# Kernel optimization log

Hardware: AMD Instinct MI355X
Metric: run time of the kernel (lower is better)

## Reference

```python
import jax, jax.numpy as jnp
import numpy as np

B, T, C_IN, H, W = 4, 3, 64, 64, 64
E = 96            # embed_dim
K = 3             # patch_size / deformable kernel size
PAD = 1
N = K * K         # 9 sampled positions per pixel
TOPK = 2
DG = 8            # deformable groups


def conv3x3(x, w, b):
    y = jax.lax.conv_general_dilated(x, w, (1, 1), ((1, 1), (1, 1)),
                                     dimension_numbers=('NCHW', 'OIHW', 'NCHW'))
    return y + b[None, :, None, None]


def lrelu(x):
    return jnp.where(x >= 0, x, 0.1 * x)


def deform_sample(x, off_feat, om_w, om_b):
    """DSP_sep2: modulated deformable sampling. Returns (B, C, N, H, W)."""
    B_, C, H_, W_ = x.shape
    om = conv3x3(off_feat, om_w, om_b).reshape(B_, 3, DG, N, H_, W_)
    off_y, off_x, mask = om[:, 0], om[:, 1], jax.nn.sigmoid(om[:, 2])  # (B,DG,N,H,W)
    ky = (jnp.arange(N) // K - PAD).astype(x.dtype)
    kx = (jnp.arange(N) % K - PAD).astype(x.dtype)
    py = off_y + ky[None, None, :, None, None] + jnp.arange(H_, dtype=x.dtype)[None, None, None, :, None]
    px = off_x + kx[None, None, :, None, None] + jnp.arange(W_, dtype=x.dtype)[None, None, None, None, :]
    y0 = jnp.floor(py); x0 = jnp.floor(px)
    wy = py - y0;       wx = px - x0
    xg = x.reshape(B_, DG, C // DG, H_, W_)
    gat = jax.vmap(jax.vmap(lambda xg_, yi, xi: xg_[:, yi, xi]))  # -> (B,DG,Cg,N,H,W)

    def corner(yc, xc, wgt):
        valid = ((yc >= 0) & (yc < H_) & (xc >= 0) & (xc < W_)).astype(x.dtype)
        yi = jnp.clip(yc, 0, H_ - 1).astype(jnp.int32)
        xi = jnp.clip(xc, 0, W_ - 1).astype(jnp.int32)
        return gat(xg, yi, xi) * (wgt * valid)[:, :, None]

    out = (corner(y0,     x0,     (1 - wy) * (1 - wx)) +
           corner(y0,     x0 + 1, (1 - wy) * wx) +
           corner(y0 + 1, x0,     wy * (1 - wx)) +
           corner(y0 + 1, x0 + 1, wy * wx))
    out = out * mask[:, :, None]  # modulation
    return out.reshape(B_, C, N, H_, W_)


def deform_attn(q, k, v, oc1_w, oc1_b, oc2_w, oc2_b, om_w, om_b):
    B_, E_, H_, W_ = q.shape
    HW = H_ * W_
    off = lrelu(conv3x3(jnp.concatenate([q, k], axis=1), oc1_w, oc1_b))
    off = lrelu(conv3x3(off, oc2_w, oc2_b))
    ko = deform_sample(k, off, om_w, om_b).transpose(0, 3, 4, 2, 1).reshape(B_, HW, N, E_)
    vo = deform_sample(v, off, om_w, om_b).transpose(0, 3, 4, 2, 1).reshape(B_, HW, N, E_)
    qr = q.reshape(B_, E_, HW).transpose(0, 2, 1)              # (B,HW,E)
    rel = jnp.einsum('bpne,bpe->bpn', ko, qr)                  # (B,HW,N)
    vals, idx = jax.lax.top_k(rel, TOPK)                       # (B,HW,k)
    corr = jax.nn.softmax(vals, axis=-1)
    idx_e = jnp.broadcast_to(idx[..., None], idx.shape + (E_,))
    ksel = jnp.take_along_axis(ko, idx_e, axis=2)              # (B,HW,k,E)
    vsel = jnp.take_along_axis(vo, idx_e, axis=2)
    k_up = jnp.einsum('bpke,bpk->bpe', ksel, corr)
    w_ori = jnp.einsum('bpe,bpe->bp', qr, k_up)                # (B,HW)
    v_re = jnp.einsum('bpke,bpk->bpe', vsel, corr).transpose(0, 2, 1)  # (B,E,HW)
    return w_ori, v_re


def setup_inputs() -> dict:
    key = jax.random.key(0)
    ks = jax.random.split(key, 18)
    s = 0.05
    return {
        'fea_full_map': jax.random.normal(ks[0], (B, T, C_IN, H, W), jnp.float32),
        'cf_w': s * jax.random.normal(ks[1], (E, C_IN, 3, 3), jnp.float32),
        'cf_b': s * jax.random.normal(ks[2], (E,), jnp.float32),
        'wq':   s * jax.random.normal(ks[3], (E, E), jnp.float32),
        'bq':   s * jax.random.normal(ks[4], (E,), jnp.float32),
        'wk':   s * jax.random.normal(ks[5], (E, E), jnp.float32),
        'bk':   s * jax.random.normal(ks[6], (E,), jnp.float32),
        'wv':   s * jax.random.normal(ks[7], (E, E), jnp.float32),
        'bv':   s * jax.random.normal(ks[8], (E,), jnp.float32),
        'oc1_w': s * jax.random.normal(ks[9], (E, 2 * E, 3, 3), jnp.float32),
        'oc1_b': s * jax.random.normal(ks[10], (E,), jnp.float32),
        'oc2_w': s * jax.random.normal(ks[11], (E, E, 3, 3), jnp.float32),
        'oc2_b': s * jax.random.normal(ks[12], (E,), jnp.float32),
        'om_w': 0.01 * jax.random.normal(ks[13], (DG * 3 * N, E, 3, 3), jnp.float32),
        'om_b': 0.01 * jax.random.normal(ks[14], (DG * 3 * N,), jnp.float32),
        'cl_w': s * jax.random.normal(ks[15], (C_IN, E, 3, 3), jnp.float32),
        'cl_b': s * jax.random.normal(ks[16], (C_IN,), jnp.float32),
    }


def reference(fea_full_map, cf_w, cf_b, wq, bq, wk, bk, wv, bv,
              oc1_w, oc1_b, oc2_w, oc2_b, om_w, om_b, cl_w, cl_b):
    B_, T_, C_, H_, W_ = fea_full_map.shape
    x = fea_full_map.reshape(B_ * T_, C_, H_, W_)
    emb = conv3x3(x, cf_w, cf_b).reshape(B_, T_, E, H_, W_)
    # per-frame linear Q/K/V over the channel dim (nn.Linear: y = x W^T + b)
    q = jnp.einsum('btchw,dc->btdhw', emb, wq) + bq[None, None, :, None, None]
    k = jnp.einsum('btchw,dc->btdhw', emb, wk) + bk[None, None, :, None, None]
    v = jnp.einsum('btchw,dc->btdhw', emb, wv) + bv[None, None, :, None, None]
    feats = []
    for jj in range(T_):
        ws, vs = [], []
        for ii in range(T_):
            if ii != jj:
                w_, v_ = deform_attn(q[:, jj], k[:, ii], v[:, ii],
                                     oc1_w, oc1_b, oc2_w, oc2_b, om_w, om_b)
                ws.append(w_); vs.append(v_)
        wm = jax.nn.softmax(jnp.stack(ws, axis=1), axis=1)  # (B, T-1, HW)
        vm = jnp.stack(vs, axis=1)                          # (B, T-1, E, HW)
        feats.append((vm * wm[:, :, None, :]).sum(axis=1).reshape(B_, E, H_, W_))
    f = jnp.stack(feats, axis=1).reshape(B_ * T_, E, H_, W_)
    out = conv3x3(f, cl_w, cl_b)
    return out + x
```

## Files before the change

### kernel.cpp

```cpp
#include <hip/hip_runtime.h>
#include <math.h>

#define PIXN 4096

typedef _Float16 f16;
typedef short s16x8 __attribute__((ext_vector_type(8)));
typedef unsigned short u16x4 __attribute__((ext_vector_type(4)));
typedef float f32x4 __attribute__((ext_vector_type(4)));

__device__ __forceinline__ f16 f2h(float f) { return (f16)f; }
__device__ __forceinline__ float h2f(f16 h) { return (float)h; }

__device__ __forceinline__ unsigned short f2bf(float f) {
  unsigned u = __float_as_uint(f);
  u += 0x7fffu + ((u >> 16) & 1u);
  return (unsigned short)(u >> 16);
}
__device__ __forceinline__ float bf2f(unsigned short h) {
  return __uint_as_float(((unsigned)h) << 16);
}

enum { ACT_NONE = 0, ACT_LRELU = 1, ACT_SIG144 = 2 };
enum { IN_FLAT = 1, IN_UVPAIR = 2, IN_QKV = 3, IN_BF = 4 };
enum { OUT_FLAT = 0, OUT_NCHWRES = 1 };

__device__ __forceinline__ void wprep_mfma(const float* __restrict__ w, unsigned short* __restrict__ dst,
                                           int srcCIN, int cinOff, int COUTv, int COUTP,
                                           int total, int idx) {
  if (idx >= total) return;
  int e = idx & 7;
  int t = idx >> 3;
  int co = t % COUTP; t /= COUTP;
  int kch = t & 3; t >>= 2;
  int KCv = srcCIN == 64 ? 2 : 3;
  (void)KCv;
  int kc = t % 3;
  int tap = t / 3;
  int ci = kc * 32 + kch * 8 + e;
  float v = 0.f;
  if (co < COUTv) v = w[((long)co * srcCIN + cinOff + ci) * 9 + tap];
  unsigned short h = f2bf(v);
  dst[idx] = h;
  dst[total + idx] = f2bf(v - bf2f(h));
}

__global__ __launch_bounds__(256) void prep_all(
    const float* __restrict__ cf_w, const float* __restrict__ oc1_w,
    const float* __restrict__ oc2_w, const float* __restrict__ om_w,
    const float* __restrict__ cl_w,
    const float* __restrict__ wq, const float* __restrict__ wk, const float* __restrict__ wv,
    const float* __restrict__ bq, const float* __restrict__ bk, const float* __restrict__ bv,
    const float* __restrict__ cf_b,
    unsigned short* __restrict__ WBQ, float* __restrict__ BQ,
    unsigned short* __restrict__ WB1, unsigned short* __restrict__ WB2,
    unsigned short* __restrict__ WB3, unsigned short* __restrict__ WB4) {
  int idx = blockIdx.x * 256 + threadIdx.x;
  switch (blockIdx.y) {
    case 0: {
      if (idx < 288) {
        int m = idx / 96, ep = idx % 96;
        const float* wm = (m == 0) ? wq : (m == 1) ? wk : wv;
        const float* bm = (m == 0) ? bq : (m == 1) ? bk : bv;
        float s = bm[ep];
        for (int c = 0; c < 96; ++c) s = fmaf(wm[ep * 96 + c], cf_b[c], s);
        BQ[idx] = s;
      }
      if (idx < 165888) {
        int e = idx & 7;
        int t = idx >> 3;
        int co = t % 288; t /= 288;
        int kch = t & 3; t >>= 2;
        int kc = t & 1, tap = t >> 1;
        int ci = kc * 32 + kch * 8 + e;
        int m = co / 96, ep = co % 96;
        const float* wm = (m == 0) ? wq : (m == 1) ? wk : wv;
        float s = 0.f;
        for (int c = 0; c < 96; ++c)
          s = fmaf(wm[ep * 96 + c], cf_w[((long)c * 64 + ci) * 9 + tap], s);
        unsigned short h = f2bf(s);
        WBQ[idx] = h;
        WBQ[165888 + idx] = f2bf(s - bf2f(h));
      }
      break;
    }
    case 1: wprep_mfma(oc1_w, WB1, 192, 0, 96, 96, 82944, idx); break;
    case 2: wprep_mfma(oc1_w, WB1 + 2 * 82944, 192, 96, 96, 96, 82944, idx); break;
    case 3: wprep_mfma(oc2_w, WB2, 96, 0, 96, 96, 82944, idx); break;
    case 4: wprep_mfma(om_w, WB3, 96, 0, 216, 224, 193536, idx); break;
    default: wprep_mfma(cl_w, WB4, 96, 0, 64, 64, 55296, idx); break;
  }
}

__global__ __launch_bounds__(256) void nchw2bf(const float* __restrict__ fea,
                                               unsigned short* __restrict__ hi,
                                               unsigned short* __restrict__ lo) {
  const int y = blockIdx.x;
  const int img = blockIdx.y;
  const int t = threadIdx.x;
  const int x = t & 63, cg = t >> 6;
  __shared__ unsigned short sh[64][68], sl[64][68];
  const float* base = fea + ((long)img * 64) * PIXN + y * 64;
#pragma unroll
  for (int k = 0; k < 16; ++k) {
    int ci = cg * 16 + k;
    float v = base[(long)ci * PIXN + x];
    unsigned short h = f2bf(v);
    sh[x][ci] = h;
    sl[x][ci] = f2bf(v - bf2f(h));
  }
  __syncthreads();
  const long ob = (long)img * PIXN + y * 64;
  for (int i = t; i < 2048; i += 256) {
    int plane = i >> 10;
    int r = i & 1023;
    int px = r >> 4, q4 = r & 15;
    u16x4 v4 = *reinterpret_cast<const u16x4*>(plane ? &sl[px][q4 * 4] : &sh[px][q4 * 4]);
    unsigned short* dst = (plane ? lo : hi) + (ob + px) * 64 + q4 * 4;
    *reinterpret_cast<u16x4*>(dst) = v4;
  }
}

template <int CIN, int COUT, int COUTW, int NCOG, int IMODE, int ACT, int OMODE>
__global__ __launch_bounds__(512, 4) void conv3x3r(
    const float* __restrict__ in, const float* __restrict__ in2,
    const float* __restrict__ bias_in,
    const unsigned short* __restrict__ WB,
    const float* __restrict__ bias,
    float* __restrict__ out,
    const float* __restrict__ resid) {
  constexpr int KC = CIN / 32;
  constexpr int COG = COUTW / NCOG;
  constexpr int NTW = COG / 32;
  constexpr int AST = 4 * 66 * 8 + 8;
  constexpr int APL = 4 * AST;
  constexpr int BSTEP = COUTW * 32;
  constexpr int TOTB = 9 * KC * BSTEP;

  __shared__ __align__(16) unsigned short Abuf[2 * APL];

  const int tid = threadIdx.x;
  const int lane = tid & 63;
  const int wid = tid >> 6;
  const int wm = wid & 3;
  const int wn = wid >> 2;
  const int iz = blockIdx.y;
  const int y0 = blockIdx.x * 2;
  const int zoff = (NCOG > 1) ? blockIdx.z * COG : 0;

  const float* baseA = nullptr;
  const float* baseB2 = nullptr;
  const unsigned short* hpl = nullptr;
  const unsigned short* lpl = nullptr;
  const unsigned short* wbe = WB;
  int LDV = CIN;
  if constexpr (IMODE == IN_UVPAIR) {
    int pair = iz >> 2, b = iz & 3;
    int jj = pair >> 1, rr2 = pair & 1;
    int ii = (rr2 == 0) ? (jj == 0 ? 1 : 0) : (jj == 2 ? 1 : 2);
    baseA = in + (long)(b * 3 + jj) * (PIXN * 96);
    baseB2 = in2 + (long)(b * 3 + ii) * (PIXN * 96);
    LDV = 96;
  } else if constexpr (IMODE == IN_QKV) {
    int sel = iz / 12, img = iz % 12;
    baseA = in + (long)img * (PIXN * 288) + sel * 96;
    wbe = WB + (long)sel * (2 * TOTB);
    LDV = 288;
  } else if constexpr (IMODE == IN_BF) {
    hpl = reinterpret_cast<const unsigned short*>(in) + (long)iz * (PIXN * 64);
    lpl = reinterpret_cast<const unsigned short*>(in2) + (long)iz * (PIXN * 64);
  } else {
    baseA = in + (long)iz * ((long)PIXN * CIN);
    LDV = CIN;
  }

  auto stageA = [&](int kc) {
    if constexpr (IMODE == IN_BF) {
      for (int i = tid; i < 4 * 66 * 4; i += 512) {
        int ci8 = i & 3;
        int t = i >> 2;
        int xp = t % 66, rr = t / 66;
        int y = y0 + rr - 1, x = xp - 1;
        s16x8 hv = {0, 0, 0, 0, 0, 0, 0, 0};
        s16x8 lv = {0, 0, 0, 0, 0, 0, 0, 0};
        if ((unsigned)y < 64u && (unsigned)x < 64u) {
          long off = (long)(y * 64 + x) * 64 + kc * 32 + ci8 * 8;
          hv = *reinterpret_cast<const s16x8*>(hpl + off);
          lv = *reinterpret_cast<const s16x8*>(lpl + off);
        }
        int base = ci8 * AST + (rr * 66 + xp) * 8;
        *reinterpret_cast<s16x8*>(&Abuf[base]) = hv;
        *reinterpret_cast<s16x8*>(&Abuf[APL + base]) = lv;
      }
    } else {
      for (int i = tid; i < 4 * 66 * 8; i += 512) {
        int ci4 = i & 7;
        int t = i >> 3;
        int xp = t % 66, rr = t / 66;
        int y = y0 + rr - 1, x = xp - 1;
        float4 v = make_float4(0.f, 0.f, 0.f, 0.f);
        if ((unsigned)y < 64u && (unsigned)x < 64u) {
          long off = (long)(y * 64 + x) * LDV + kc * 32 + ci4 * 4;
          if constexpr (IMODE == IN_UVPAIR) {
            float4 u = *reinterpret_cast<const float4*>(baseA + off);
            float4 w2 = *reinterpret_cast<const float4*>(baseB2 + off);
            float4 bi = *reinterpret_cast<const float4*>(bias_in + kc * 32 + ci4 * 4);
            v.x = u.x + w2.x + bi.x; v.x = v.x >= 0.f ? v.x : 0.1f * v.x;
            v.y = u.y + w2.y + bi.y; v.y = v.y >= 0.f ? v.y : 0.1f * v.y;
            v.z = u.z + w2.z + bi.z; v.z = v.z >= 0.f ? v.z : 0.1f * v.z;
            v.w = u.w + w2.w + bi.w; v.w = v.w >= 0.f ? v.w : 0.1f * v.w;
          } else {
            v = *reinterpret_cast<const float4*>(baseA + off);
          }
        }
        unsigned short h0 = f2bf(v.x), h1 = f2bf(v.y), h2 = f2bf(v.z), h3 = f2bf(v.w);
        u16x4 hv = {h0, h1, h2, h3};
        u16x4 lv = {f2bf(v.x - bf2f(h0)), f2bf(v.y - bf2f(h1)),
                    f2bf(v.z - bf2f(h2)), f2bf(v.w - bf2f(h3))};
        int base = (ci4 >> 1) * AST + (rr * 66 + xp) * 8 + (ci4 & 1) * 4;
        *reinterpret_cast<u16x4*>(&Abuf[base]) = hv;
        *reinterpret_cast<u16x4*>(&Abuf[APL + base]) = lv;
      }
    }
  };

  f32x4 acc[2][NTW];
#pragma unroll
  for (int nt = 0; nt < NTW; ++nt) {
    int co = zoff + (wn * NTW + nt) * 16 + (lane & 15);
    float b0 = 0.f;
    if (bias != nullptr && co < COUT) b0 = bias[co];
#pragma unroll
    for (int mt2 = 0; mt2 < 2; ++mt2) {
      acc[mt2][nt][0] = b0; acc[mt2][nt][1] = b0;
      acc[mt2][nt][2] = b0; acc[mt2][nt][3] = b0;
    }
  }

  stageA(0);
  __syncthreads();

  const int blo = ((lane >> 4) * COUTW + zoff + (wn * NTW) * 16 + (lane & 15)) * 8;

  s16x8 b0h, b0l, b1h, b1l;
  {
    const unsigned short* p = wbe + blo;
    b0h = *reinterpret_cast<const s16x8*>(p);
    b0l = *reinterpret_cast<const s16x8*>(p + TOTB);
  }

  long bo = 0;
#pragma unroll 1
  for (int kc = 0; kc < KC; ++kc) {
#pragma unroll 1
    for (int tap = 0; tap < 9; ++tap) {
      const int dy = tap / 3, dx = tap % 3;
      const long bo_next = (tap < 8) ? bo + (long)KC * BSTEP
                                     : ((kc + 1 < KC) ? (long)(kc + 1) * BSTEP : 0);

      s16x8 ah[2], al[2];
      {
        int ci8 = lane >> 4;
        int m = lane & 15;
#pragma unroll
        for (int mt2 = 0; mt2 < 2; ++mt2) {
          int px = (wm * 2 + mt2) * 16 + m;
          int r = px >> 6, x = px & 63;
          int aoff = ci8 * AST + ((r + dy) * 66 + (x + dx)) * 8;
          ah[mt2] = *reinterpret_cast<const s16x8*>(&Abuf[aoff]);
          al[mt2] = *reinterpret_cast<const s16x8*>(&Abuf[APL + aoff]);
        }
      }

#pragma unroll
      for (int nt = 0; nt < NTW; ++nt) {
        const long nboff = (nt + 1 < NTW) ? (bo + (long)(nt + 1) * 128) : bo_next;
        const unsigned short* np = wbe + nboff + blo;
        if ((nt & 1) == 0) {
          b1h = *reinterpret_cast<const s16x8*>(np);
          b1l = *reinterpret_cast<const s16x8*>(np + TOTB);
        } else {
          b0h = *reinterpret_cast<const s16x8*>(np);
          b0l = *reinterpret_cast<const s16x8*>(np + TOTB);
        }
        const s16x8 bh = (nt & 1) ? b1h : b0h;
        const s16x8 bl = (nt & 1) ? b1l : b0l;
#pragma unroll
        for (int mt2 = 0; mt2 < 2; ++mt2) {
          acc[mt2][nt] = __builtin_amdgcn_mfma_f32_16x16x32_bf16(ah[mt2], bh, acc[mt2][nt], 0, 0, 0);
          acc[mt2][nt] = __builtin_amdgcn_mfma_f32_16x16x32_bf16(al[mt2], bh, acc[mt2][nt], 0, 0, 0);
          acc[mt2][nt] = __builtin_amdgcn_mfma_f32_16x16x32_bf16(ah[mt2], bl, acc[mt2][nt], 0, 0, 0);
        }
      }
      if constexpr (NTW & 1) {
        b0h = b1h; b0l = b1l;
      }
      bo = bo_next;
    }
    if (kc + 1 < KC) {
      __syncthreads();
      stageA(kc + 1);
      __syncthreads();
    }
  }

#pragma unroll
  for (int mt2 = 0; mt2 < 2; ++mt2) {
#pragma unroll
    for (int nt = 0; nt < NTW; ++nt) {
      int co = zoff + (wn * NTW + nt) * 16 + (lane & 15);
      if (COUTW > COUT && co >= COUT) continue;
#pragma unroll
      for (int r = 0; r < 4; ++r) {
        int px = (wm * 2 + mt2) * 16 + (lane >> 4) * 4 + r;
        float v = acc[mt2][nt][r];
        if constexpr (ACT == ACT_LRELU) v = v >= 0.f ? v : 0.1f * v;
        if constexpr (ACT == ACT_SIG144) {
          if (co >= 144) v = 1.f / (1.f + expf(-v));
        }
        if constexpr (OMODE == OUT_FLAT) {
          const long obase = (long)iz * PIXN + blockIdx.x * 128;
          out[(obase + px) * COUT + co] = v;
        } else {
          long oo = (long)iz * ((long)COUT * PIXN) + (long)co * PIXN + blockIdx.x * 128 + px;
          out[oo] = v + resid[oo];
        }
      }
    }
  }
}

#define CWSLOT 580
__global__ __launch_bounds__(256) void attn3_k(const float* __restrict__ qkv,
                                               const float* __restrict__ om,
                                               float* __restrict__ w_buf,
                                               f16* __restrict__ vre) {
  const int pair = blockIdx.y;
  const int jj = pair >> 1, rr = pair & 1;
  const int ii = (rr == 0) ? (jj == 0 ? 1 : 0) : (jj == 2 ? 1 : 2);
  const int wv = threadIdx.x >> 6;
  const int lane = threadIdx.x & 63;
  const int bp0 = blockIdx.x * 8 + wv * 2;

  __shared__ float s_om[8 * 216];
  __shared__ float s_cw[8 * CWSLOT];

  {
    const float* omrow = om + ((long)pair * 16384 + bp0) * 216;
    float* dst = s_om + wv * 432;
    for (int i = lane; i < 432; i += 64) dst[i] = omrow[i];
  }
  __syncthreads();

  for (int t = lane; t < 144; t += 64) {
    int ph = t / 72, cmb = t - ph * 72;
    int g = cmb / 9, n = cmb - g * 9;
    int p = (bp0 + ph) & 4095;
    int y = p >> 6, x = p & 63;
    const float* so = s_om + (wv * 2 + ph) * 216;
    float oy = so[g * 9 + n], ox = so[72 + g * 9 + n], m = so[144 + g * 9 + n];
    float py = oy + (float)(y + n / 3 - 1);
    float px = ox + (float)(x + n % 3 - 1);
    float y0f = floorf(py), x0f = floorf(px);
    float wy = py - y0f, wx = px - x0f;
    float* dst = s_cw + (wv * 2 + ph) * CWSLOT + cmb * 8;
#pragma unroll
    for (int dy = 0; dy < 2; ++dy) {
#pragma unroll
      for (int dx = 0; dx < 2; ++dx) {
        float yc = y0f + dy, xc = x0f + dx;
        bool valid = (yc >= 0.f) & (yc < 64.f) & (xc >= 0.f) & (xc < 64.f);
        float w = (dy ? wy : 1.f - wy) * (dx ? wx : 1.f - wx) * m;
        w = valid ? w : 0.f;
        int yi = (int)fminf(fmaxf(yc, 0.f), 63.f);
        int xi = (int)fminf(fmaxf(xc, 0.f), 63.f);
        int idx = (yi * 64 + xi) * 288 + 96;
        dst[dy * 2 + dx] = w;
        dst[4 + dy * 2 + dx] = __int_as_float(idx);
      }
    }
  }
  __syncthreads();

  const int ph = lane >> 5;
  const int li = lane & 31;
  const int bp = bp0 + ph;
  const int b = bp >> 12;
  const int cb = li * 3;
  const int g = li >> 2;
  const float* kimg = qkv + (long)(b * 3 + ii) * (PIXN * 288);
  const float* qrow = qkv + ((long)(b * 3 + jj) * PIXN + (bp & 4095)) * 288 + cb;
  const float q0 = qrow[0], q1 = qrow[1], q2 = qrow[2];
  const float* cw = s_cw + (wv * 2 + ph) * CWSLOT + g * 9 * 8;

  float ka[9][3];
  float rel[9];
#pragma unroll
  for (int n = 0; n < 9; ++n) {
    float4 w4 = *reinterpret_cast<const float4*>(cw + n * 8);
    float4 i4 = *reinterpret_cast<const float4*>(cw + n * 8 + 4);
    int ia = __float_as_int(i4.x) + cb, ib = __float_as_int(i4.y) + cb;
    int ic = __float_as_int(i4.z) + cb, id = __float_as_int(i4.w) + cb;
#pragma unroll
    for (int j = 0; j < 3; ++j) {
      float a = w4.x * kimg[ia + j];
      a = fmaf(w4.y, kimg[ib + j], a);
      a = fmaf(w4.z, kimg[ic + j], a);
      a = fmaf(w4.w, kimg[id + j], a);
      ka[n][j] = a;
    }
    float part = q0 * ka[n][0];
    part = fmaf(q1, ka[n][1], part);
    part = fmaf(q2, ka[n][2], part);
#pragma unroll
    for (int off = 16; off > 0; off >>= 1) part += __shfl_xor(part, off, 64);
    rel[n] = part;
  }

  int i0 = 0; float v0 = rel[0];
  float ks0a = ka[0][0], ks0b = ka[0][1], ks0c = ka[0][2];
#pragma unroll
  for (int n = 1; n < 9; ++n) {
    bool t = rel[n] > v0;
    v0 = t ? rel[n] : v0; i0 = t ? n : i0;
    ks0a = t ? ka[n][0] : ks0a; ks0b = t ? ka[n][1] : ks0b; ks0c = t ? ka[n][2] : ks0c;
  }
  int i1 = 0; float v1 = -3.4e38f;
  float ks1a = 0.f, ks1b = 0.f, ks1c = 0.f;
#pragma unroll
  for (int n = 0; n < 9; ++n) {
    bool t = (n != i0) && rel[n] > v1;
    v1 = t ? rel[n] : v1; i1 = t ? n : i1;
    ks1a = t ? ka[n][0] : ks1a; ks1b = t ? ka[n][1] : ks1b; ks1c = t ? ka[n][2] : ks1c;
  }
  float e = expf(v1 - v0);
  float cw0 = 1.f / (1.f + e), cw1 = e * cw0;

  float wpart = q0 * (cw0 * ks0a + cw1 * ks1a);
  wpart = fmaf(q1, cw0 * ks0b + cw1 * ks1b, wpart);
  wpart = fmaf(q2, cw0 * ks0c + cw1 * ks1c, wpart);
#pragma unroll
  for (int off = 16; off > 0; off >>= 1) wpart += __shfl_xor(wpart, off, 64);
  if (li == 0) w_buf[(long)pair * 16384 + bp] = wpart;

  float4 wA = *reinterpret_cast<const float4*>(cw + i0 * 8);
  float4 iA = *reinterpret_cast<const float4*>(cw + i0 * 8 + 4);
  float4 wB = *reinterpret_cast<const float4*>(cw + i1 * 8);
  float4 iB = *reinterpret_cast<const float4*>(cw + i1 * 8 + 4);
  int a0 = __float_as_int(iA.x) + 96 + cb, a1 = __float_as_int(iA.y) + 96 + cb;
  int a2 = __float_as_int(iA.z) + 96 + cb, a3 = __float_as_int(iA.w) + 96 + cb;
  int b0 = __float_as_int(iB.x) + 96 + cb, b1 = __float_as_int(iB.y) + 96 + cb;
  int b2 = __float_as_int(iB.z) + 96 + cb, b3 = __float_as_int(iB.w) + 96 + cb;
  f16* vrow = vre + ((long)pair * 16384 + bp) * 96 + cb;
#pragma unroll
  for (int j = 0; j < 3; ++j) {
    float va = wA.x * kimg[a0 + j];
    va = fmaf(wA.y, kimg[a1 + j], va);
    va = fmaf(wA.z, kimg[a2 + j], va);
    va = fmaf(wA.w, kimg[a3 + j], va);
    float vb = wB.x * kimg[b0 + j];
    vb = fmaf(wB.y, kimg[b1 + j], vb);
    vb = fmaf(wB.z, kimg[b2 + j], vb);
    vb = fmaf(wB.w, kimg[b3 + j], vb);
    vrow[j] = f2h(cw0 * va + cw1 * vb);
  }
}

__global__ __launch_bounds__(256) void merge_k(const float* __restrict__ w_buf,
                                               const f16* __restrict__ vre,
                                               float* __restrict__ f_t) {
  long idx = (long)blockIdx.x * 256 + threadIdx.x;
  const long TOT = (long)4 * 3 * PIXN * 24;
  if (idx >= TOT) return;
  int c4 = idx % 24;
  long t = idx / 24;
  int p = t % PIXN;
  long t2 = t / PIXN;
  int jj = t2 % 3;
  int b = (int)(t2 / 3);
  long bpi = (long)b * PIXN + p;
  int pr0 = jj * 2, pr1 = jj * 2 + 1;
  float w0 = w_buf[(long)pr0 * 16384 + bpi];
  float w1 = w_buf[(long)pr1 * 16384 + bpi];
  float mx = fmaxf(w0, w1);
  float e0 = expf(w0 - mx), e1 = expf(w1 - mx);
  float inv = 1.f / (e0 + e1);
  float s0 = e0 * inv, s1 = e1 * inv;
  const f16* va = &vre[((long)pr0 * 16384 + bpi) * 96 + c4 * 4];
  const f16* vb = &vre[((long)pr1 * 16384 + bpi) * 96 + c4 * 4];
  float4 r;
  r.x = s0 * h2f(va[0]) + s1 * h2f(vb[0]);
  r.y = s0 * h2f(va[1]) + s1 * h2f(vb[1]);
  r.z = s0 * h2f(va[2]) + s1 * h2f(vb[2]);
  r.w = s0 * h2f(va[3]) + s1 * h2f(vb[3]);
  *reinterpret_cast<float4*>(f_t + ((long)(b * 3 + jj) * PIXN + p) * 96 + c4 * 4) = r;
}

extern "C" void kernel_launch(void* const* d_in, const int* in_sizes, int n_in,
                              void* d_out, int out_size, void* d_ws, size_t ws_size,
                              hipStream_t stream) {
  const float* fea = (const float*)d_in[0];
  const float* cf_w = (const float*)d_in[1];
  const float* cf_b = (const float*)d_in[2];
  const float* wq = (const float*)d_in[3];
  const float* bq = (const float*)d_in[4];
  const float* wk = (const float*)d_in[5];
  const float* bk = (const float*)d_in[6];
  const float* wv = (const float*)d_in[7];
  const float* bv = (const float*)d_in[8];
  const float* oc1_w = (const float*)d_in[9];
  const float* oc1_b = (const float*)d_in[10];
  const float* oc2_w = (const float*)d_in[11];
  const float* oc2_b = (const float*)d_in[12];
  const float* om_w = (const float*)d_in[13];
  const float* om_b = (const float*)d_in[14];
  const float* cl_w = (const float*)d_in[15];
  const float* cl_b = (const float*)d_in[16];

  char* base = (char*)d_ws;
  size_t o = 0;
  auto carve = [&](size_t bytes) { char* p = base + o; o += (bytes + 255) & ~255UL; return p; };

  unsigned short* WBQ = (unsigned short*)carve(2UL * 165888 * 2);
  float* BQ = (float*)carve(288UL * 4);
  unsigned short* WB1 = (unsigned short*)carve(2UL * 2 * 82944 * 2);
  unsigned short* WB2 = (unsigned short*)carve(2UL * 82944 * 2);
  unsigned short* WB3 = (unsigned short*)carve(2UL * 193536 * 2);
  unsigned short* WB4 = (unsigned short*)carve(2UL * 55296 * 2);
  unsigned short* feaH = (unsigned short*)carve(12UL * PIXN * 64 * 2);
  unsigned short* feaL = (unsigned short*)carve(12UL * PIXN * 64 * 2);

  float* om_t = (float*)carve(21233664UL * 4);
  float* qkv_t = (float*)carve(14155776UL * 4);
  float* U_t = (float*)carve(4718592UL * 4);
  float* V_t = (float*)carve(4718592UL * 4);
  float* off2_t = (float*)carve(9437184UL * 4);
  float* w_buf = (float*)carve(98304UL * 4);
  float* f_t = U_t;
  f16* vre_b = (f16*)V_t;

  prep_all<<<dim3(756, 6), 256, 0, stream>>>(cf_w, oc1_w, oc2_w, om_w, cl_w,
                                             wq, wk, wv, bq, bk, bv, cf_b,
                                             WBQ, BQ, WB1, WB2, WB3, WB4);

  nchw2bf<<<dim3(64, 12), 256, 0, stream>>>(fea, feaH, feaL);

  conv3x3r<64, 288, 288, 3, IN_BF, ACT_NONE, OUT_FLAT><<<dim3(32, 12, 3), 512, 0, stream>>>(
      (const float*)feaH, (const float*)feaL, nullptr, WBQ, BQ, qkv_t, nullptr);

  conv3x3r<96, 96, 96, 1, IN_QKV, ACT_NONE, OUT_FLAT><<<dim3(32, 24, 1), 512, 0, stream>>>(
      qkv_t, nullptr, nullptr, WB1, nullptr, U_t, nullptr);

  conv3x3r<96, 96, 96, 1, IN_UVPAIR, ACT_LRELU, OUT_FLAT><<<dim3(32, 24, 1), 512, 0, stream>>>(
      U_t, V_t, oc1_b, WB2, oc2_b, off2_t, nullptr);

  conv3x3r<96, 216, 224, 1, IN_FLAT, ACT_SIG144, OUT_FLAT><<<dim3(32, 24, 1), 512, 0, stream>>>(
      off2_t, nullptr, nullptr, WB3, om_b, om_t, nullptr);

  attn3_k<<<dim3(2048, 6), 256, 0, stream>>>(qkv_t, om_t, w_buf, vre_b);
  merge_k<<<4608, 256, 0, stream>>>(w_buf, vre_b, f_t);

  conv3x3r<96, 64, 64, 1, IN_FLAT, ACT_NONE, OUT_NCHWRES><<<dim3(32, 12, 1), 512, 0, stream>>>(
      f_t, nullptr, nullptr, WB4, cl_b, (float*)d_out, fea);
}
```

Measured before the change: 515.9 us.

## Parameterize conv warp layout and split offset-mask conv across output-channel groups

Adds a WN template parameter that sets how the 8 waves split pixels versus output channels, so each wave handles WN pixel tiles and a matching number of channel tiles. Weight fragments for the next tap are now prefetched into a per-tile register array for the whole tap instead of ping-ponging one tile ahead. The offset/mask conv pads its output channels to 256, splits them into two z-groups and uses a 4x4 wave layout, doubling its grid so more blocks run concurrently. The costs are extra padded weight traffic and more registers for the prefetched B fragments, which could lower occupancy.

```diff
diff --git a/kernel.cpp b/kernel.cpp
--- a/kernel.cpp
+++ b/kernel.cpp
@@ -32,8 +32,6 @@
   int t = idx >> 3;
   int co = t % COUTP; t /= COUTP;
   int kch = t & 3; t >>= 2;
-  int KCv = srcCIN == 64 ? 2 : 3;
-  (void)KCv;
   int kc = t % 3;
   int tap = t / 3;
   int ci = kc * 32 + kch * 8 + e;
@@ -86,7 +84,7 @@
     case 1: wprep_mfma(oc1_w, WB1, 192, 0, 96, 96, 82944, idx); break;
     case 2: wprep_mfma(oc1_w, WB1 + 2 * 82944, 192, 96, 96, 96, 82944, idx); break;
     case 3: wprep_mfma(oc2_w, WB2, 96, 0, 96, 96, 82944, idx); break;
-    case 4: wprep_mfma(om_w, WB3, 96, 0, 216, 224, 193536, idx); break;
+    case 4: wprep_mfma(om_w, WB3, 96, 0, 216, 256, 221184, idx); break;
     default: wprep_mfma(cl_w, WB4, 96, 0, 64, 64, 55296, idx); break;
   }
 }
@@ -120,7 +118,7 @@
   }
 }
 
-template <int CIN, int COUT, int COUTW, int NCOG, int IMODE, int ACT, int OMODE>
+template <int CIN, int COUT, int COUTW, int NCOG, int IMODE, int ACT, int OMODE, int WN>
 __global__ __launch_bounds__(512, 4) void conv3x3r(
     const float* __restrict__ in, const float* __restrict__ in2,
     const float* __restrict__ bias_in,
@@ -129,8 +127,10 @@
     float* __restrict__ out,
     const float* __restrict__ resid) {
   constexpr int KC = CIN / 32;
+  constexpr int WM = 8 / WN;
+  constexpr int MT = WN;
   constexpr int COG = COUTW / NCOG;
-  constexpr int NTW = COG / 32;
+  constexpr int NTW = COG / (WN * 16);
   constexpr int AST = 4 * 66 * 8 + 8;
   constexpr int APL = 4 * AST;
   constexpr int BSTEP = COUTW * 32;
@@ -141,8 +141,8 @@
   const int tid = threadIdx.x;
   const int lane = tid & 63;
   const int wid = tid >> 6;
-  const int wm = wid & 3;
-  const int wn = wid >> 2;
+  const int wm = wid % WM;
+  const int wn = wid / WM;
   const int iz = blockIdx.y;
   const int y0 = blockIdx.x * 2;
   const int zoff = (NCOG > 1) ? blockIdx.z * COG : 0;
@@ -223,16 +223,16 @@
     }
   };
 
-  f32x4 acc[2][NTW];
+  f32x4 acc[MT][NTW];
 #pragma unroll
   for (int nt = 0; nt < NTW; ++nt) {
     int co = zoff + (wn * NTW + nt) * 16 + (lane & 15);
     float b0 = 0.f;
     if (bias != nullptr && co < COUT) b0 = bias[co];
 #pragma unroll
-    for (int mt2 = 0; mt2 < 2; ++mt2) {
-      acc[mt2][nt][0] = b0; acc[mt2][nt][1] = b0;
-      acc[mt2][nt][2] = b0; acc[mt2][nt][3] = b0;
+    for (int mt = 0; mt < MT; ++mt) {
+      acc[mt][nt][0] = b0; acc[mt][nt][1] = b0;
+      acc[mt][nt][2] = b0; acc[mt][nt][3] = b0;
     }
   }
 
@@ -241,11 +241,12 @@
 
   const int blo = ((lane >> 4) * COUTW + zoff + (wn * NTW) * 16 + (lane & 15)) * 8;
 
-  s16x8 b0h, b0l, b1h, b1l;
-  {
-    const unsigned short* p = wbe + blo;
-    b0h = *reinterpret_cast<const s16x8*>(p);
-    b0l = *reinterpret_cast<const s16x8*>(p + TOTB);
+  s16x8 cbh[NTW], cbl[NTW], pbh[NTW], pbl[NTW];
+#pragma unroll
+  for (int nt = 0; nt < NTW; ++nt) {
+    const unsigned short* p = wbe + (long)nt * 128 + blo;
+    pbh[nt] = *reinterpret_cast<const s16x8*>(p);
+    pbl[nt] = *reinterpret_cast<const s16x8*>(p + TOTB);
   }
 
   long bo = 0;
@@ -254,45 +255,42 @@
 #pragma unroll 1
     for (int tap = 0; tap < 9; ++tap) {
       const int dy = tap / 3, dx = tap % 3;
-      const long bo_next = (tap < 8) ? bo + (long)KC * BSTEP
-                                     : ((kc + 1 < KC) ? (long)(kc + 1) * BSTEP : 0);
-
-      s16x8 ah[2], al[2];
+      const bool last = (kc == KC - 1) && (tap == 8);
+      const long bo_next = (tap < 8) ? bo + (long)KC * BSTEP : (long)(kc + 1) * BSTEP;
+
+#pragma unroll
+      for (int nt = 0; nt < NTW; ++nt) { cbh[nt] = pbh[nt]; cbl[nt] = pbl[nt]; }
+      if (!last) {
+#pragma unroll
+        for (int nt = 0; nt < NTW; ++nt) {
+          const unsigned short* np = wbe + bo_next + (long)nt * 128 + blo;
+          pbh[nt] = *reinterpret_cast<const s16x8*>(np);
+          pbl[nt] = *reinterpret_cast<const s16x8*>(np + TOTB);
+        }
+      }
+
+      s16x8 ah[MT], al[MT];
       {
         int ci8 = lane >> 4;
         int m = lane & 15;
 #pragma unroll
-        for (int mt2 = 0; mt2 < 2; ++mt2) {
-          int px = (wm * 2 + mt2) * 16 + m;
+        for (int mt = 0; mt < MT; ++mt) {
+          int px = (wm * MT + mt) * 16 + m;
           int r = px >> 6, x = px & 63;
           int aoff = ci8 * AST + ((r + dy) * 66 + (x + dx)) * 8;
-          ah[mt2] = *reinterpret_cast<const s16x8*>(&Abuf[aoff]);
-          al[mt2] = *reinterpret_cast<const s16x8*>(&Abuf[APL + aoff]);
+          ah[mt] = *reinterpret_cast<const s16x8*>(&Abuf[aoff]);
+          al[mt] = *reinterpret_cast<const s16x8*>(&Abuf[APL + aoff]);
         }
       }
 
 #pragma unroll
       for (int nt = 0; nt < NTW; ++nt) {
-        const long nboff = (nt + 1 < NTW) ? (bo + (long)(nt + 1) * 128) : bo_next;
-        const unsigned short* np = wbe + nboff + blo;
-        if ((nt & 1) == 0) {
-          b1h = *reinterpret_cast<const s16x8*>(np);
-          b1l = *reinterpret_cast<const s16x8*>(np + TOTB);
-        } else {
-          b0h = *reinterpret_cast<const s16x8*>(np);
-          b0l = *reinterpret_cast<const s16x8*>(np + TOTB);
-        }
-        const s16x8 bh = (nt & 1) ? b1h : b0h;
-        const s16x8 bl = (nt & 1) ? b1l : b0l;
-#pragma unroll
-        for (int mt2 = 0; mt2 < 2; ++mt2) {
-          acc[mt2][nt] = __builtin_amdgcn_mfma_f32_16x16x32_bf16(ah[mt2], bh, acc[mt2][nt], 0, 0, 0);
-          acc[mt2][nt] = __builtin_amdgcn_mfma_f32_16x16x32_bf16(al[mt2], bh, acc[mt2][nt], 0, 0, 0);
-          acc[mt2][nt] = __builtin_amdgcn_mfma_f32_16x16x32_bf16(ah[mt2], bl, acc[mt2][nt], 0, 0, 0);
-        }
-      }
-      if constexpr (NTW & 1) {
-        b0h = b1h; b0l = b1l;
+#pragma unroll
+        for (int mt = 0; mt < MT; ++mt) {
+          acc[mt][nt] = __builtin_amdgcn_mfma_f32_16x16x32_bf16(ah[mt], cbh[nt], acc[mt][nt], 0, 0, 0);
+          acc[mt][nt] = __builtin_amdgcn_mfma_f32_16x16x32_bf16(al[mt], cbh[nt], acc[mt][nt], 0, 0, 0);
+          acc[mt][nt] = __builtin_amdgcn_mfma_f32_16x16x32_bf16(ah[mt], cbl[nt], acc[mt][nt], 0, 0, 0);
+        }
       }
       bo = bo_next;
     }
@@ -304,15 +302,15 @@
   }
 
 #pragma unroll
-  for (int mt2 = 0; mt2 < 2; ++mt2) {
+  for (int mt = 0; mt < MT; ++mt) {
 #pragma unroll
     for (int nt = 0; nt < NTW; ++nt) {
       int co = zoff + (wn * NTW + nt) * 16 + (lane & 15);
       if (COUTW > COUT && co >= COUT) continue;
 #pragma unroll
       for (int r = 0; r < 4; ++r) {
-        int px = (wm * 2 + mt2) * 16 + (lane >> 4) * 4 + r;
-        float v = acc[mt2][nt][r];
+        int px = (wm * MT + mt) * 16 + (lane >> 4) * 4 + r;
+        float v = acc[mt][nt][r];
         if constexpr (ACT == ACT_LRELU) v = v >= 0.f ? v : 0.1f * v;
         if constexpr (ACT == ACT_SIG144) {
           if (co >= 144) v = 1.f / (1.f + expf(-v));
@@ -524,7 +522,7 @@
   float* BQ = (float*)carve(288UL * 4);
   unsigned short* WB1 = (unsigned short*)carve(2UL * 2 * 82944 * 2);
   unsigned short* WB2 = (unsigned short*)carve(2UL * 82944 * 2);
-  unsigned short* WB3 = (unsigned short*)carve(2UL * 193536 * 2);
+  unsigned short* WB3 = (unsigned short*)carve(2UL * 221184 * 2);
   unsigned short* WB4 = (unsigned short*)carve(2UL * 55296 * 2);
   unsigned short* feaH = (unsigned short*)carve(12UL * PIXN * 64 * 2);
   unsigned short* feaL = (unsigned short*)carve(12UL * PIXN * 64 * 2);
@@ -538,27 +536,27 @@
   float* f_t = U_t;
   f16* vre_b = (f16*)V_t;
 
-  prep_all<<<dim3(756, 6), 256, 0, stream>>>(cf_w, oc1_w, oc2_w, om_w, cl_w,
+  prep_all<<<dim3(864, 6), 256, 0, stream>>>(cf_w, oc1_w, oc2_w, om_w, cl_w,
                                              wq, wk, wv, bq, bk, bv, cf_b,
                                              WBQ, BQ, WB1, WB2, WB3, WB4);
 
   nchw2bf<<<dim3(64, 12), 256, 0, stream>>>(fea, feaH, feaL);
 
-  conv3x3r<64, 288, 288, 3, IN_BF, ACT_NONE, OUT_FLAT><<<dim3(32, 12, 3), 512, 0, stream>>>(
+  conv3x3r<64, 288, 288, 3, IN_BF, ACT_NONE, OUT_FLAT, 2><<<dim3(32, 12, 3), 512, 0, stream>>>(
       (const float*)feaH, (const float*)feaL, nullptr, WBQ, BQ, qkv_t, nullptr);
 
-  conv3x3r<96, 96, 96, 1, IN_QKV, ACT_NONE, OUT_FLAT><<<dim3(32, 24, 1), 512, 0, stream>>>(
+  conv3x3r<96, 96, 96, 1, IN_QKV, ACT_NONE, OUT_FLAT, 2><<<dim3(32, 24, 1), 512, 0, stream>>>(
       qkv_t, nullptr, nullptr, WB1, nullptr, U_t, nullptr);
 
-  conv3x3r<96, 96, 96, 1, IN_UVPAIR, ACT_LRELU, OUT_FLAT><<<dim3(32, 24, 1), 512, 0, stream>>>(
+  conv3x3r<96, 96, 96, 1, IN_UVPAIR, ACT_LRELU, OUT_FLAT, 2><<<dim3(32, 24, 1), 512, 0, stream>>>(
       U_t, V_t, oc1_b, WB2, oc2_b, off2_t, nullptr);
 
-  conv3x3r<96, 216, 224, 1, IN_FLAT, ACT_SIG144, OUT_FLAT><<<dim3(32, 24, 1), 512, 0, stream>>>(
+  conv3x3r<96, 216, 256, 2, IN_FLAT, ACT_SIG144, OUT_FLAT, 4><<<dim3(32, 24, 2), 512, 0, stream>>>(
       off2_t, nullptr, nullptr, WB3, om_b, om_t, nullptr);
 
   attn3_k<<<dim3(2048, 6), 256, 0, stream>>>(qkv_t, om_t, w_buf, vre_b);
   merge_k<<<4608, 256, 0, stream>>>(w_buf, vre_b, f_t);
 
-  conv3x3r<96, 64, 64, 1, IN_FLAT, ACT_NONE, OUT_NCHWRES><<<dim3(32, 12, 1), 512, 0, stream>>>(
+  conv3x3r<96, 64, 64, 1, IN_FLAT, ACT_NONE, OUT_NCHWRES, 2><<<dim3(32, 12, 1), 512, 0, stream>>>(
       f_t, nullptr, nullptr, WB4, cl_b, (float*)d_out, fea);
 }
```

New measurement: 491.6 us. 1.05x faster.
